# Kernel optimization log

Measured on AMD Instinct MI355X. Metric: run time of the kernel, lower is better.

The kernel has to match this reference:

```python
import jax, jax.numpy as jnp
import numpy as np

B, S, D = 2, 2048, 2048
H = 16
HD = D // H  # 128
ROPE_THETA = 10000.0
NEG_INF = -1e9


def _rope_tables(seqlen, head_dim):
    inv = 1.0 / (ROPE_THETA ** (np.arange(0, head_dim, 2, dtype=np.float32) / head_dim))
    t = np.arange(seqlen, dtype=np.float32)
    freqs = np.outer(t, inv)  # (S, HD/2)
    return jnp.asarray(np.cos(freqs)), jnp.asarray(np.sin(freqs))


def _apply_rope(x, cos, sin):
    # x: (B, S, H, HD); cos/sin: (S, HD/2) -> complex multiply on (even, odd) pairs
    x = x.reshape(*x.shape[:-1], HD // 2, 2)
    x0, x1 = x[..., 0], x[..., 1]
    c = cos[None, :, None, :]
    s = sin[None, :, None, :]
    o0 = x0 * c - x1 * s
    o1 = x0 * s + x1 * c
    return jnp.stack([o0, o1], axis=-1).reshape(*x.shape[:-2], HD)


def setup_inputs() -> dict:
    key = jax.random.key(0)
    ks = jax.random.split(key, 6)
    std = 1.0 / np.sqrt(D)
    x = jax.random.normal(ks[0], (B, S, D), dtype=jnp.float32)
    wq = jax.random.normal(ks[1], (D, D), dtype=jnp.float32) * std
    wk = jax.random.normal(ks[2], (D, D), dtype=jnp.float32) * std
    wv = jax.random.normal(ks[3], (D, D), dtype=jnp.float32) * std
    wo = jax.random.normal(ks[4], (D, D), dtype=jnp.float32) * std
    cos, sin = _rope_tables(S, HD)
    # additive causal mask
    mask = jnp.where(jnp.tril(jnp.ones((S, S), dtype=bool)), 0.0, NEG_INF).astype(jnp.float32)
    return {"x": x, "wq": wq, "wk": wk, "wv": wv, "wo": wo, "cos": cos, "sin": sin, "mask": mask, "start_p": 0}


def reference(x, wq, wk, wv, wo, cos, sin, mask, start_p):
    bsz, seqlen, _ = x.shape
    xq = (x @ wq.T).reshape(bsz, seqlen, H, HD)
    xk = (x @ wk.T).reshape(bsz, seqlen, H, HD)
    xv = (x @ wv.T).reshape(bsz, seqlen, H, HD)
    c = cos[start_p:start_p + seqlen]
    s = sin[start_p:start_p + seqlen]
    xq = _apply_rope(xq, c, s)
    xk = _apply_rope(xk, c, s)
    # (B, H, S, HD)
    q = xq.transpose(0, 2, 1, 3)
    k = xk.transpose(0, 2, 1, 3)
    v = xv.transpose(0, 2, 1, 3)
    scores = jnp.einsum("bhqd,bhkd->bhqk", q, k) / np.sqrt(HD).astype(np.float32)
    scores = scores + mask[None, None, :, :]
    probs = jax.nn.softmax(scores.astype(jnp.float32), axis=-1).astype(q.dtype)
    out = jnp.einsum("bhqk,bhkd->bhqd", probs, v)
    out = out.transpose(0, 2, 1, 3).reshape(bsz, seqlen, H * HD)
    return out @ wo.T
```

## Files before the change

kernel.cpp:

```cpp
#include <hip/hip_runtime.h>
#include <cstdint>
#include <cstddef>

typedef unsigned short u16;
typedef unsigned int u32;
typedef __attribute__((ext_vector_type(8))) short short8;
typedef __attribute__((ext_vector_type(2))) unsigned int u32x2;
typedef __attribute__((ext_vector_type(8))) __bf16 bf16x8;
typedef __attribute__((ext_vector_type(4))) float f32x4;

#define BB 2
#define SS 2048
#define DD 2048
#define HH 16
#define HD 128

__device__ __forceinline__ u16 f2bf(float x) {
  u32 u = __float_as_uint(x);
  u32 r = (u + 0x7FFFu + ((u >> 16) & 1u)) >> 16;
  return (u16)r;
}
__device__ __forceinline__ float bf2f(u16 h) {
  return __uint_as_float(((u32)h) << 16);
}
__device__ __forceinline__ float exp2_hw(float x) {
  return __builtin_amdgcn_exp2f(x);
}
__device__ __forceinline__ u32 cvtpk_bf16(float lo, float hi) {
  u32 r;
  asm("v_cvt_pk_bf16_f32 %0, %1, %2" : "=v"(r) : "v"(lo), "v"(hi));
  return r;
}

__device__ __forceinline__ f32x4 mfma16x16x32(short8 a, short8 b, f32x4 c) {
  return __builtin_amdgcn_mfma_f32_16x16x32_bf16(
      __builtin_bit_cast(bf16x8, a), __builtin_bit_cast(bf16x8, b), c, 0, 0, 0);
}

__device__ __forceinline__ void gload_lds16(const void* g, void* l) {
  __builtin_amdgcn_global_load_lds(
      (const __attribute__((address_space(1))) void*)g,
      (__attribute__((address_space(3))) void*)l, 16, 0, 0);
}

__global__ void cast_kernel(const float* __restrict__ src, u16* __restrict__ dst, int n8) {
  int i = blockIdx.x * blockDim.x + threadIdx.x;
  if (i >= n8) return;
  const float* s = src + (size_t)i * 8;
  f32x4 a = *reinterpret_cast<const f32x4*>(s);
  f32x4 b = *reinterpret_cast<const f32x4*>(s + 4);
  short8 o;
  o[0] = (short)f2bf(a[0]); o[1] = (short)f2bf(a[1]);
  o[2] = (short)f2bf(a[2]); o[3] = (short)f2bf(a[3]);
  o[4] = (short)f2bf(b[0]); o[5] = (short)f2bf(b[1]);
  o[6] = (short)f2bf(b[2]); o[7] = (short)f2bf(b[3]);
  *reinterpret_cast<short8*>(dst + (size_t)i * 8) = o;
}

template <int OUTF32>
__global__ __launch_bounds__(256) void gemm_nt(const u16* __restrict__ A,
                                               const u16* __restrict__ Bw,
                                               void* __restrict__ Cout) {
  constexpr int K = 2048, N = 2048;
  __shared__ u16 As[128 * 32];
  __shared__ u16 Bs[128 * 32];
  const int t = threadIdx.x;
  const int w = t >> 6, l = t & 63;
  const int bm = blockIdx.x, bn = blockIdx.y;
  const int wm = (w >> 1) * 64, wn = (w & 1) * 64;
  const int lr = l & 15, lg = l >> 4;
  f32x4 acc[4][4] = {};

  for (int kk = 0; kk < K; kk += 32) {
    __syncthreads();
#pragma unroll
    for (int i = 0; i < 2; ++i) {
      int cb = (i * 4 + w) * 64;
      int chunk = cb + l;
      int row = chunk >> 2, kc = chunk & 3;
      gload_lds16(A + (size_t)(bm * 128 + row) * K + kk + kc * 8, (u16*)As + cb * 8);
      gload_lds16(Bw + (size_t)(bn * 128 + row) * K + kk + kc * 8, (u16*)Bs + cb * 8);
    }
    __syncthreads();
    short8 af[4], bf[4];
#pragma unroll
    for (int mi = 0; mi < 4; ++mi)
      af[mi] = *reinterpret_cast<const short8*>(&As[(wm + mi * 16 + lr) * 32 + lg * 8]);
#pragma unroll
    for (int ni = 0; ni < 4; ++ni)
      bf[ni] = *reinterpret_cast<const short8*>(&Bs[(wn + ni * 16 + lr) * 32 + lg * 8]);
#pragma unroll
    for (int mi = 0; mi < 4; ++mi)
#pragma unroll
      for (int ni = 0; ni < 4; ++ni)
        acc[mi][ni] = mfma16x16x32(af[mi], bf[ni], acc[mi][ni]);
  }
#pragma unroll
  for (int mi = 0; mi < 4; ++mi)
#pragma unroll
    for (int ni = 0; ni < 4; ++ni)
#pragma unroll
      for (int r = 0; r < 4; ++r) {
        int row = bm * 128 + wm + mi * 16 + lg * 4 + r;
        int col = bn * 128 + wn + ni * 16 + lr;
        float v = acc[mi][ni][r];
        if (OUTF32)
          ((float*)Cout)[(size_t)row * N + col] = v;
        else
          ((u16*)Cout)[(size_t)row * N + col] = f2bf(v);
      }
}

__global__ void rope_kernel(u32* __restrict__ XQ, u32* __restrict__ XK,
                            const float* __restrict__ cosT, const float* __restrict__ sinT) {
  int p = blockIdx.x * blockDim.x + threadIdx.x;
  int i = p & 63;
  int s = (p >> 10) & (SS - 1);
  float c = cosT[s * 64 + i], sn = sinT[s * 64 + i];
  u32 q = XQ[p], k = XK[p];
  float q0 = bf2f((u16)(q & 0xFFFF)), q1 = bf2f((u16)(q >> 16));
  float k0 = bf2f((u16)(k & 0xFFFF)), k1 = bf2f((u16)(k >> 16));
  float oq0 = q0 * c - q1 * sn, oq1 = q0 * sn + q1 * c;
  float ok0 = k0 * c - k1 * sn, ok1 = k0 * sn + k1 * c;
  XQ[p] = (u32)f2bf(oq0) | ((u32)f2bf(oq1) << 16);
  XK[p] = (u32)f2bf(ok0) | ((u32)f2bf(ok1) << 16);
}

__global__ __launch_bounds__(512, 2) void attn_kernel(const u16* __restrict__ XQ,
                                                      const u16* __restrict__ XK,
                                                      const u16* __restrict__ XV,
                                                      u16* __restrict__ AO) {
  __shared__ u16 Ks[2][64 * 128];
  __shared__ u16 Vs[2][128 * 64];
  __shared__ u16 Ps[8][16 * 64];
  const int ib = blockIdx.x, bh = blockIdx.y;
  const int b = bh >> 4, h = bh & 15;
  const int t = threadIdx.x, w = t >> 6, l = t & 63;
  const int wh = w >> 2, wl = w & 3;
  const int lr = l & 15, lg = l >> 4;
  const int qtA = 2 * ib + wh;
  const int qtB = 31 - 2 * ib - wh;
  const int qbA = qtA * 64 + wl * 16;
  const int qbB = qtB * 64 + wl * 16;
  const int nkv = 32 - 2 * ib;
  const size_t rowbase = (size_t)b * SS;

  const short one_bf = (short)0x3F80;
  const short8 onesf = {one_bf, one_bf, one_bf, one_bf, one_bf, one_bf, one_bf, one_bf};

  short8 qfA[4], qfB[4];
  {
    const u16* qpA = XQ + (rowbase + qbA + lr) * DD + h * HD + lg * 8;
    const u16* qpB = XQ + (rowbase + qbB + lr) * DD + h * HD + lg * 8;
#pragma unroll
    for (int ks = 0; ks < 4; ++ks) {
      qfA[ks] = *reinterpret_cast<const short8*>(qpA + ks * 32);
      qfB[ks] = *reinterpret_cast<const short8*>(qpB + ks * 32);
    }
  }

  f32x4 oA[8] = {}, oB[8] = {};
  f32x4 lsA = {}, lsB = {};
  float mrA = -1e30f, mrB = -1e30f;

  char* Pw = (char*)Ps[w];
  short8 vr[2];
  const int vk0 = (t >> 4) * 2;
  const int vd0 = (t & 15) * 8;

  auto issueK = [&](int kvt, int buf) {
#pragma unroll
    for (int i2 = 0; i2 < 2; ++i2) {
      int cb = (w * 2 + i2) * 64;
      int chunk = cb + l;
      int krow = chunk >> 4, kc = chunk & 15;
      int lc = kc ^ (krow & 7);
      gload_lds16(XK + (rowbase + kvt * 64 + krow) * DD + h * HD + lc * 8,
                  (u16*)Ks[buf] + cb * 8);
    }
  };
  auto loadV = [&](int kvt) {
    const u16* vp = XV + (rowbase + kvt * 64 + vk0) * DD + h * HD + vd0;
    vr[0] = *reinterpret_cast<const short8*>(vp);
    vr[1] = *reinterpret_cast<const short8*>(vp + DD);
  };
  auto writeV = [&](int buf) {
    char* base = (char*)Vs[buf];
#pragma unroll
    for (int ii = 0; ii < 8; ++ii) {
      int d = vd0 + ii;
      int off = d * 128 + ((vk0 * 2) ^ ((((d >> 3) & 7) ^ (d & 7)) << 4));
      u32 pk = (u32)(u16)vr[0][ii] | ((u32)(u16)vr[1][ii] << 16);
      *reinterpret_cast<u32*>(base + off) = pk;
    }
  };

  auto softmax_pv = [&](int kv, int cur, f32x4* sf, float& mr, f32x4& lsa, f32x4* o, int qbase) {
    const float scale2 = 0.12751743f;
    const bool diag = (kv == (qbase >> 6));
    const int kv0 = kv * 64;
    float pb[4][4];
#pragma unroll
    for (int kt = 0; kt < 4; ++kt)
#pragma unroll
      for (int r = 0; r < 4; ++r) {
        float s = sf[kt][r] * scale2;
        if (diag) {
          int kg = kv0 + kt * 16 + lg * 4 + r;
          int qg = qbase + lr;
          if (kg > qg) s = -1e30f;
        }
        pb[kt][r] = s;
      }
    float lm = pb[0][0];
#pragma unroll
    for (int kt = 0; kt < 4; ++kt)
#pragma unroll
      for (int r = 0; r < 4; ++r) lm = fmaxf(lm, pb[kt][r]);
    if (__any((int)(lm > mr + 11.54f))) {
      float m = lm;
      m = fmaxf(m, __shfl_xor(m, 16));
      m = fmaxf(m, __shfl_xor(m, 32));
      float mn = fmaxf(mr, m);
      float sc = exp2_hw(mr - mn);
      mr = mn;
#pragma unroll
      for (int r = 0; r < 4; ++r) {
        float scr = __shfl(sc, (l & 48) + lg * 4 + r);
        lsa[r] *= scr;
#pragma unroll
        for (int dt = 0; dt < 8; ++dt) o[dt][r] *= scr;
      }
    }
#pragma unroll
    for (int kt = 0; kt < 4; ++kt)
#pragma unroll
      for (int r = 0; r < 4; ++r)
        pb[kt][r] = exp2_hw(pb[kt][r] - mr);
    char* Pr = Pw + lr * 128;
    const int swz = (lr & 7) << 4;
#pragma unroll
    for (int kt = 0; kt < 4; ++kt) {
      u32x2 wv;
      wv[0] = cvtpk_bf16(pb[kt][0], pb[kt][1]);
      wv[1] = cvtpk_bf16(pb[kt][2], pb[kt][3]);
      *reinterpret_cast<u32x2*>(Pr + ((kt * 32 + lg * 8) ^ swz)) = wv;
    }
    short8 pa[2];
#pragma unroll
    for (int ks = 0; ks < 2; ++ks)
      pa[ks] = *reinterpret_cast<const short8*>(Pr + ((ks * 64 + lg * 16) ^ swz));
    lsa = mfma16x16x32(pa[0], onesf, lsa);
    lsa = mfma16x16x32(pa[1], onesf, lsa);
    const char* vbase = (const char*)Vs[cur];
    __builtin_amdgcn_s_setprio(1);
#pragma unroll
    for (int dt = 0; dt < 8; ++dt)
#pragma unroll
      for (int ks = 0; ks < 2; ++ks) {
        int d = dt * 16 + lr;
        int off = d * 128 + ((ks * 64 + lg * 16) ^ ((((d >> 3) & 7) ^ (d & 7)) << 4));
        short8 vf = *reinterpret_cast<const short8*>(vbase + off);
        o[dt] = mfma16x16x32(pa[ks], vf, o[dt]);
      }
    __builtin_amdgcn_s_setprio(0);
  };

  issueK(0, 0);
  loadV(0);

  for (int kv = 0; kv < nkv; ++kv) {
    const int cur = kv & 1;
    writeV(cur);
    __syncthreads();
    if (kv + 1 < nkv) { issueK(kv + 1, cur ^ 1); loadV(kv + 1); }

    const bool doB = (kv <= qtB);
    const bool doA = (kv <= qtA);
    if (doB) {
      f32x4 sB[4], sA[4];
#pragma unroll
      for (int kt = 0; kt < 4; ++kt) {
        sB[kt] = f32x4{0.f, 0.f, 0.f, 0.f};
        sA[kt] = f32x4{0.f, 0.f, 0.f, 0.f};
      }
#pragma unroll
      for (int kt = 0; kt < 4; ++kt) {
        short8 kf[4];
#pragma unroll
        for (int ks = 0; ks < 4; ++ks) {
          int krow = kt * 16 + lr;
          int inner = (ks * 64 + lg * 16) ^ ((krow & 7) << 4);
          kf[ks] = *reinterpret_cast<const short8*>((const char*)Ks[cur] + krow * 256 + inner);
        }
#pragma unroll
        for (int ks = 0; ks < 4; ++ks) sB[kt] = mfma16x16x32(kf[ks], qfB[ks], sB[kt]);
        if (doA) {
#pragma unroll
          for (int ks = 0; ks < 4; ++ks) sA[kt] = mfma16x16x32(kf[ks], qfA[ks], sA[kt]);
        }
      }
      softmax_pv(kv, cur, sB, mrB, lsB, oB, qbB);
      if (doA) softmax_pv(kv, cur, sA, mrA, lsA, oA, qbA);
    }
  }

#pragma unroll
  for (int r = 0; r < 4; ++r) {
    float invB = 1.0f / lsB[r];
    float invA = 1.0f / lsA[r];
    int qgB = qbB + lg * 4 + r;
    int qgA = qbA + lg * 4 + r;
    u16* opB = AO + (rowbase + qgB) * DD + h * HD + lr;
    u16* opA = AO + (rowbase + qgA) * DD + h * HD + lr;
#pragma unroll
    for (int dt = 0; dt < 8; ++dt) {
      opB[dt * 16] = f2bf(oB[dt][r] * invB);
      opA[dt * 16] = f2bf(oA[dt][r] * invA);
    }
  }
}

extern "C" void kernel_launch(void* const* d_in, const int* in_sizes, int n_in,
                              void* d_out, int out_size, void* d_ws, size_t ws_size,
                              hipStream_t stream) {
  const float* x = (const float*)d_in[0];
  const float* wq = (const float*)d_in[1];
  const float* wk = (const float*)d_in[2];
  const float* wv = (const float*)d_in[3];
  const float* wo = (const float*)d_in[4];
  const float* cosT = (const float*)d_in[5];
  const float* sinT = (const float*)d_in[6];

  char* ws = (char*)d_ws;
  u16* xb  = (u16*)(ws);
  u16* wqb = (u16*)(ws + 16777216);
  u16* wkb = (u16*)(ws + 25165824);
  u16* wvb = (u16*)(ws + 33554432);
  u16* wob = (u16*)(ws + 41943040);
  u16* XQ  = (u16*)(ws + 50331648);
  u16* XK  = (u16*)(ws + 67108864);
  u16* XV  = (u16*)(ws + 83886080);
  u16* AO  = (u16*)(ws + 100663296);

  cast_kernel<<<4096, 256, 0, stream>>>(x, xb, 1048576);
  cast_kernel<<<2048, 256, 0, stream>>>(wq, wqb, 524288);
  cast_kernel<<<2048, 256, 0, stream>>>(wk, wkb, 524288);
  cast_kernel<<<2048, 256, 0, stream>>>(wv, wvb, 524288);
  cast_kernel<<<2048, 256, 0, stream>>>(wo, wob, 524288);

  dim3 gg(32, 16);
  gemm_nt<0><<<gg, 256, 0, stream>>>(xb, wqb, XQ);
  gemm_nt<0><<<gg, 256, 0, stream>>>(xb, wkb, XK);
  gemm_nt<0><<<gg, 256, 0, stream>>>(xb, wvb, XV);

  rope_kernel<<<16384, 256, 0, stream>>>((u32*)XQ, (u32*)XK, cosT, sinT);

  attn_kernel<<<dim3(8, 32), 512, 0, stream>>>(XQ, XK, XV, AO);

  gemm_nt<1><<<gg, 256, 0, stream>>>(AO, wob, d_out);
}
```

Baseline: 325.5 us.

## Fuse Q/K/V projections into one GEMM with RoPE applied in the epilogue

The three separate Q, K and V projection GEMMs become a single launch over a concatenated weight matrix. This relies on the three bf16 weight buffers already sitting contiguously in the workspace. RoPE is now applied in the GEMM epilogue, pairing adjacent columns with a lane shuffle, so the standalone rope kernel and its extra read/write pass over Q and K are gone. In exchange the epilogue does per-element cos/sin loads and a conditional, and rounding happens once instead of twice, which changes numerics slightly.

```diff
diff --git a/kernel.cpp b/kernel.cpp
--- a/kernel.cpp
+++ b/kernel.cpp
@@ -57,10 +57,9 @@
   *reinterpret_cast<short8*>(dst + (size_t)i * 8) = o;
 }
 
-template <int OUTF32>
-__global__ __launch_bounds__(256) void gemm_nt(const u16* __restrict__ A,
-                                               const u16* __restrict__ Bw,
-                                               void* __restrict__ Cout) {
+__global__ __launch_bounds__(256) void gemm_nt_f32(const u16* __restrict__ A,
+                                                   const u16* __restrict__ Bw,
+                                                   float* __restrict__ Cout) {
   constexpr int K = 2048, N = 2048;
   __shared__ u16 As[128 * 32];
   __shared__ u16 Bs[128 * 32];
@@ -103,27 +102,72 @@
       for (int r = 0; r < 4; ++r) {
         int row = bm * 128 + wm + mi * 16 + lg * 4 + r;
         int col = bn * 128 + wn + ni * 16 + lr;
+        Cout[(size_t)row * N + col] = acc[mi][ni][r];
+      }
+}
+
+__global__ __launch_bounds__(256) void gemm_qkv(const u16* __restrict__ A,
+                                                const u16* __restrict__ Bw,
+                                                u16* __restrict__ XQ,
+                                                u16* __restrict__ XK,
+                                                u16* __restrict__ XV,
+                                                const float* __restrict__ cosT,
+                                                const float* __restrict__ sinT) {
+  constexpr int K = 2048;
+  __shared__ u16 As[128 * 32];
+  __shared__ u16 Bs[128 * 32];
+  const int t = threadIdx.x;
+  const int w = t >> 6, l = t & 63;
+  const int bm = blockIdx.x, bn = blockIdx.y;
+  const int wm = (w >> 1) * 64, wn = (w & 1) * 64;
+  const int lr = l & 15, lg = l >> 4;
+  f32x4 acc[4][4] = {};
+
+  for (int kk = 0; kk < K; kk += 32) {
+    __syncthreads();
+#pragma unroll
+    for (int i = 0; i < 2; ++i) {
+      int cb = (i * 4 + w) * 64;
+      int chunk = cb + l;
+      int row = chunk >> 2, kc = chunk & 3;
+      gload_lds16(A + (size_t)(bm * 128 + row) * K + kk + kc * 8, (u16*)As + cb * 8);
+      gload_lds16(Bw + (size_t)(bn * 128 + row) * K + kk + kc * 8, (u16*)Bs + cb * 8);
+    }
+    __syncthreads();
+    short8 af[4], bf[4];
+#pragma unroll
+    for (int mi = 0; mi < 4; ++mi)
+      af[mi] = *reinterpret_cast<const short8*>(&As[(wm + mi * 16 + lr) * 32 + lg * 8]);
+#pragma unroll
+    for (int ni = 0; ni < 4; ++ni)
+      bf[ni] = *reinterpret_cast<const short8*>(&Bs[(wn + ni * 16 + lr) * 32 + lg * 8]);
+#pragma unroll
+    for (int mi = 0; mi < 4; ++mi)
+#pragma unroll
+      for (int ni = 0; ni < 4; ++ni)
+        acc[mi][ni] = mfma16x16x32(af[mi], bf[ni], acc[mi][ni]);
+  }
+
+  const int reg = bn >> 4;
+  u16* dst = (reg == 0) ? XQ : ((reg == 1) ? XK : XV);
+#pragma unroll
+  for (int mi = 0; mi < 4; ++mi)
+#pragma unroll
+    for (int ni = 0; ni < 4; ++ni)
+#pragma unroll
+      for (int r = 0; r < 4; ++r) {
+        int row = bm * 128 + wm + mi * 16 + lg * 4 + r;
+        int c = (bn * 128 + wn + ni * 16 + lr) & 2047;
         float v = acc[mi][ni][r];
-        if (OUTF32)
-          ((float*)Cout)[(size_t)row * N + col] = v;
-        else
-          ((u16*)Cout)[(size_t)row * N + col] = f2bf(v);
-      }
-}
-
-__global__ void rope_kernel(u32* __restrict__ XQ, u32* __restrict__ XK,
-                            const float* __restrict__ cosT, const float* __restrict__ sinT) {
-  int p = blockIdx.x * blockDim.x + threadIdx.x;
-  int i = p & 63;
-  int s = (p >> 10) & (SS - 1);
-  float c = cosT[s * 64 + i], sn = sinT[s * 64 + i];
-  u32 q = XQ[p], k = XK[p];
-  float q0 = bf2f((u16)(q & 0xFFFF)), q1 = bf2f((u16)(q >> 16));
-  float k0 = bf2f((u16)(k & 0xFFFF)), k1 = bf2f((u16)(k >> 16));
-  float oq0 = q0 * c - q1 * sn, oq1 = q0 * sn + q1 * c;
-  float ok0 = k0 * c - k1 * sn, ok1 = k0 * sn + k1 * c;
-  XQ[p] = (u32)f2bf(oq0) | ((u32)f2bf(oq1) << 16);
-  XK[p] = (u32)f2bf(ok0) | ((u32)f2bf(ok1) << 16);
+        if (reg < 2) {
+          float p = __shfl_xor(v, 1);
+          int s = row & (SS - 1);
+          int pi = (c & (HD - 1)) >> 1;
+          float co = cosT[s * 64 + pi], sn = sinT[s * 64 + pi];
+          v = (c & 1) ? (p * sn + v * co) : (v * co - p * sn);
+        }
+        dst[(size_t)row * 2048 + c] = f2bf(v);
+      }
 }
 
 __global__ __launch_bounds__(512, 2) void attn_kernel(const u16* __restrict__ XQ,
@@ -333,15 +377,16 @@
   const float* sinT = (const float*)d_in[6];
 
   char* ws = (char*)d_ws;
-  u16* xb  = (u16*)(ws);
-  u16* wqb = (u16*)(ws + 16777216);
-  u16* wkb = (u16*)(ws + 25165824);
-  u16* wvb = (u16*)(ws + 33554432);
-  u16* wob = (u16*)(ws + 41943040);
-  u16* XQ  = (u16*)(ws + 50331648);
-  u16* XK  = (u16*)(ws + 67108864);
-  u16* XV  = (u16*)(ws + 83886080);
-  u16* AO  = (u16*)(ws + 100663296);
+  u16* xb   = (u16*)(ws);
+  u16* wqkv = (u16*)(ws + 16777216);
+  u16* wqb  = (u16*)(ws + 16777216);
+  u16* wkb  = (u16*)(ws + 25165824);
+  u16* wvb  = (u16*)(ws + 33554432);
+  u16* wob  = (u16*)(ws + 41943040);
+  u16* XQ   = (u16*)(ws + 50331648);
+  u16* XK   = (u16*)(ws + 67108864);
+  u16* XV   = (u16*)(ws + 83886080);
+  u16* AO   = (u16*)(ws + 100663296);
 
   cast_kernel<<<4096, 256, 0, stream>>>(x, xb, 1048576);
   cast_kernel<<<2048, 256, 0, stream>>>(wq, wqb, 524288);
@@ -349,14 +394,9 @@
   cast_kernel<<<2048, 256, 0, stream>>>(wv, wvb, 524288);
   cast_kernel<<<2048, 256, 0, stream>>>(wo, wob, 524288);
 
-  dim3 gg(32, 16);
-  gemm_nt<0><<<gg, 256, 0, stream>>>(xb, wqb, XQ);
-  gemm_nt<0><<<gg, 256, 0, stream>>>(xb, wkb, XK);
-  gemm_nt<0><<<gg, 256, 0, stream>>>(xb, wvb, XV);
-
-  rope_kernel<<<16384, 256, 0, stream>>>((u32*)XQ, (u32*)XK, cosT, sinT);
+  gemm_qkv<<<dim3(32, 48), 256, 0, stream>>>(xb, wqkv, XQ, XK, XV, cosT, sinT);
 
   attn_kernel<<<dim3(8, 32), 512, 0, stream>>>(XQ, XK, XV, AO);
 
-  gemm_nt<1><<<gg, 256, 0, stream>>>(AO, wob, d_out);
-}
+  gemm_nt_f32<<<dim3(32, 16), 256, 0, stream>>>(AO, wob, (float*)d_out);
+}
```

New measurement: 349.9 us. +7.5%, slower.

## Fuse RoPE into QK projection GEMM epilogue and enlarge GEMM tiles to 256x128

Applied to the files above, without the earlier changes.

Removes the standalone RoPE kernel and applies the rotation inside the Q/K projection GEMM epilogue. The partner element of each (even, odd) pair comes from the neighbouring lane via a lane shuffle, and the rotation runs in fp32 before the bf16 store. Separately, the GEMM is widened to a 256x128 output tile with 512 threads. That halves the block count and doubles reuse of the B-operand tile per block. The intent is to drop the extra read/write pass over Q and K and cut global traffic per flop, at the cost of a single wave of 256 blocks and more per-block LDS.

```diff
diff --git a/kernel.cpp b/kernel.cpp
--- a/kernel.cpp
+++ b/kernel.cpp
@@ -57,12 +57,14 @@
   *reinterpret_cast<short8*>(dst + (size_t)i * 8) = o;
 }
 
-template <int OUTF32>
-__global__ __launch_bounds__(256) void gemm_nt(const u16* __restrict__ A,
+template <int MODE>
+__global__ __launch_bounds__(512) void gemm256(const u16* __restrict__ A,
                                                const u16* __restrict__ Bw,
-                                               void* __restrict__ Cout) {
+                                               void* __restrict__ Cout,
+                                               const float* __restrict__ cosT,
+                                               const float* __restrict__ sinT) {
   constexpr int K = 2048, N = 2048;
-  __shared__ u16 As[128 * 32];
+  __shared__ u16 As[256 * 32];
   __shared__ u16 Bs[128 * 32];
   const int t = threadIdx.x;
   const int w = t >> 6, l = t & 63;
@@ -75,10 +77,15 @@
     __syncthreads();
 #pragma unroll
     for (int i = 0; i < 2; ++i) {
-      int cb = (i * 4 + w) * 64;
+      int cb = (i * 8 + w) * 64;
       int chunk = cb + l;
       int row = chunk >> 2, kc = chunk & 3;
-      gload_lds16(A + (size_t)(bm * 128 + row) * K + kk + kc * 8, (u16*)As + cb * 8);
+      gload_lds16(A + (size_t)(bm * 256 + row) * K + kk + kc * 8, (u16*)As + cb * 8);
+    }
+    {
+      int cb = w * 64;
+      int chunk = cb + l;
+      int row = chunk >> 2, kc = chunk & 3;
       gload_lds16(Bw + (size_t)(bn * 128 + row) * K + kk + kc * 8, (u16*)Bs + cb * 8);
     }
     __syncthreads();
@@ -101,29 +108,21 @@
     for (int ni = 0; ni < 4; ++ni)
 #pragma unroll
       for (int r = 0; r < 4; ++r) {
-        int row = bm * 128 + wm + mi * 16 + lg * 4 + r;
+        int row = bm * 256 + wm + mi * 16 + lg * 4 + r;
         int col = bn * 128 + wn + ni * 16 + lr;
         float v = acc[mi][ni][r];
-        if (OUTF32)
+        if (MODE == 2) {
+          float p = __shfl_xor(v, 1);
+          int s = row & (SS - 1);
+          int pi = (col & (HD - 1)) >> 1;
+          float co = cosT[s * 64 + pi], sn = sinT[s * 64 + pi];
+          v = (col & 1) ? (p * sn + v * co) : (v * co - p * sn);
+        }
+        if (MODE == 1)
           ((float*)Cout)[(size_t)row * N + col] = v;
         else
           ((u16*)Cout)[(size_t)row * N + col] = f2bf(v);
       }
-}
-
-__global__ void rope_kernel(u32* __restrict__ XQ, u32* __restrict__ XK,
-                            const float* __restrict__ cosT, const float* __restrict__ sinT) {
-  int p = blockIdx.x * blockDim.x + threadIdx.x;
-  int i = p & 63;
-  int s = (p >> 10) & (SS - 1);
-  float c = cosT[s * 64 + i], sn = sinT[s * 64 + i];
-  u32 q = XQ[p], k = XK[p];
-  float q0 = bf2f((u16)(q & 0xFFFF)), q1 = bf2f((u16)(q >> 16));
-  float k0 = bf2f((u16)(k & 0xFFFF)), k1 = bf2f((u16)(k >> 16));
-  float oq0 = q0 * c - q1 * sn, oq1 = q0 * sn + q1 * c;
-  float ok0 = k0 * c - k1 * sn, ok1 = k0 * sn + k1 * c;
-  XQ[p] = (u32)f2bf(oq0) | ((u32)f2bf(oq1) << 16);
-  XK[p] = (u32)f2bf(ok0) | ((u32)f2bf(ok1) << 16);
 }
 
 __global__ __launch_bounds__(512, 2) void attn_kernel(const u16* __restrict__ XQ,
@@ -349,14 +348,12 @@
   cast_kernel<<<2048, 256, 0, stream>>>(wv, wvb, 524288);
   cast_kernel<<<2048, 256, 0, stream>>>(wo, wob, 524288);
 
-  dim3 gg(32, 16);
-  gemm_nt<0><<<gg, 256, 0, stream>>>(xb, wqb, XQ);
-  gemm_nt<0><<<gg, 256, 0, stream>>>(xb, wkb, XK);
-  gemm_nt<0><<<gg, 256, 0, stream>>>(xb, wvb, XV);
-
-  rope_kernel<<<16384, 256, 0, stream>>>((u32*)XQ, (u32*)XK, cosT, sinT);
+  dim3 gg(16, 16);
+  gemm256<2><<<gg, 512, 0, stream>>>(xb, wqb, XQ, cosT, sinT);
+  gemm256<2><<<gg, 512, 0, stream>>>(xb, wkb, XK, cosT, sinT);
+  gemm256<0><<<gg, 512, 0, stream>>>(xb, wvb, XV, nullptr, nullptr);
 
   attn_kernel<<<dim3(8, 32), 512, 0, stream>>>(XQ, XK, XV, AO);
 
-  gemm_nt<1><<<gg, 256, 0, stream>>>(AO, wob, d_out);
-}
+  gemm256<1><<<gg, 512, 0, stream>>>(AO, wob, d_out, nullptr, nullptr);
+}
```

New measurement: 364.5 us. 12.0% more time.
